# Optimization experiments

Measured on AMD Instinct MI355X. Metric: run time of the kernel, lower is better.

The kernel has to match this reference:

```python
import jax, jax.numpy as jnp
import numpy as np

N_HEAD = 16


def setup_inputs() -> dict:
    key = jax.random.key(0)
    ks = jax.random.split(key, 4)
    B, S, E = 1, 4096, 1024
    x = jax.random.normal(ks[0], (B, S, E), dtype=jnp.float32)
    # causal mask: True where attention is DISALLOWED (upper triangle)
    masked_matrix = ~jnp.tril(jnp.ones((S, S), dtype=bool))[None, None]
    Wqkv = jax.random.normal(ks[1], (E, 3 * E), dtype=jnp.float32) * (1.0 / np.sqrt(E))
    bqkv = jnp.zeros((3 * E,), dtype=jnp.float32)
    Wp = jax.random.normal(ks[2], (E, E), dtype=jnp.float32) * (1.0 / np.sqrt(E))
    bp = jnp.zeros((E,), dtype=jnp.float32)
    return {"x": x, "masked_matrix": masked_matrix, "Wqkv": Wqkv, "bqkv": bqkv,
            "Wp": Wp, "bp": bp}


def reference(x, masked_matrix, Wqkv, bqkv, Wp, bp):
    B, S, E = x.shape
    H = N_HEAD
    D = E // H
    qkv = x @ Wqkv + bqkv                        # [B,S,3E]
    q, k, v = jnp.split(qkv, 3, axis=-1)
    q = q.reshape(B, S, H, D).transpose(0, 2, 1, 3)  # [B,H,S,D]
    k = k.reshape(B, S, H, D).transpose(0, 2, 1, 3)
    v = v.reshape(B, S, H, D).transpose(0, 2, 1, 3)
    # NOTE: source applies NO 1/sqrt(D) scaling — kept faithful.
    att = jnp.einsum('bhqd,bhkd->bhqk', q, k)    # [B,H,S,S]
    att = jnp.where(masked_matrix, jnp.float32(-jnp.inf), att)
    att = jax.nn.softmax(att, axis=-1)
    res = jnp.einsum('bhqk,bhkd->bhqd', att, v)  # [B,H,S,D]
    res = res.transpose(0, 2, 1, 3).reshape(B, S, E)
    return res @ Wp + bp
```

## Files before the change

kernel.cpp:

```cpp
#include <hip/hip_runtime.h>
#include <hip/hip_bf16.h>
#include <math.h>

#define S_LEN 4096
#define EMB   1024
#define NHEAD 16
#define HDIM  64

typedef __attribute__((ext_vector_type(8))) _Float16 half8;
typedef __attribute__((ext_vector_type(4))) _Float16 half4;
typedef __attribute__((ext_vector_type(4))) float float4_t;
typedef __attribute__((ext_vector_type(16))) float float16_t;
typedef __attribute__((ext_vector_type(4))) int int4_t;
typedef __attribute__((ext_vector_type(2))) int int2_t;

#define GLOBAL_AS(p) ((const __attribute__((address_space(1))) void*)(p))
#define LDS_AS(p)    ((__attribute__((address_space(3))) void*)(p))

#define LOG2E 1.4426950408889634f

__global__ __launch_bounds__(256) void prep(
    const float* __restrict__ x, const float* __restrict__ Wqkv,
    const float* __restrict__ Wp,
    _Float16* __restrict__ xh, _Float16* __restrict__ WTh,
    _Float16* __restrict__ WpT)
{
    const int bid = blockIdx.x;
    if (bid < 4096) {
        const int i = bid * 256 + threadIdx.x;
        const float4_t v = ((const float4_t*)x)[i];
        half4 hh;
#pragma unroll
        for (int j = 0; j < 4; ++j) hh[j] = (_Float16)v[j];
        ((half4*)xh)[i] = hh;
        return;
    }
    __shared__ float t[64][65];
    const float* in;
    _Float16* out;
    int R, C, bx, by;
    if (bid < 4096 + 768) {
        const int idx = bid - 4096;
        bx = idx % 48; by = idx / 48;
        in = Wqkv; out = WTh; R = 1024; C = 3072;
    } else {
        const int idx = bid - 4864;
        bx = idx & 15; by = idx >> 4;
        in = Wp; out = WpT; R = 1024; C = 1024;
    }
    const int r0 = by * 64, c0 = bx * 64;
    for (int i = threadIdx.x; i < 64 * 64; i += 256) {
        int r = i >> 6, c = i & 63;
        t[r][c] = in[(size_t)(r0 + r) * C + c0 + c];
    }
    __syncthreads();
    for (int i = threadIdx.x; i < 64 * 64; i += 256) {
        int c = i >> 6, r = i & 63;
        out[(size_t)(c0 + c) * R + r0 + r] = (_Float16)t[r][c];
    }
}

__global__ __launch_bounds__(256) void gemm_qkv(
    const _Float16* __restrict__ Ag, const _Float16* __restrict__ Bg,
    const float* __restrict__ bias,
    _Float16* __restrict__ qk, _Float16* __restrict__ vt, int K)
{
    constexpr int BK = 32;
    __shared__ _Float16 Ah[128 * BK];
    __shared__ _Float16 Bh[128 * BK];

    const int tid = threadIdx.x;
    const int wave = tid >> 6, lane = tid & 63;
    const int l16 = lane & 15, quad = lane >> 4;
    const int wr = wave >> 1, wc = wave & 1;
    const int row0 = blockIdx.y * 128, col0 = blockIdx.x * 128;
    const int lrow = lane >> 2, lc8 = (lane & 3) * 8;

    float4_t acc[4][4];
#pragma unroll
    for (int i = 0; i < 4; ++i)
#pragma unroll
        for (int j = 0; j < 4; ++j) acc[i][j] = (float4_t){0.f, 0.f, 0.f, 0.f};

    for (int k0 = 0; k0 < K; k0 += BK) {
        __syncthreads();
#pragma unroll
        for (int i = 0; i < 2; ++i) {
            const int ar = i * 64 + wave * 16;
            __builtin_amdgcn_global_load_lds(
                GLOBAL_AS(Ag + (size_t)(row0 + ar + lrow) * K + k0 + lc8),
                LDS_AS(&Ah[ar * BK]), 16, 0, 0);
            __builtin_amdgcn_global_load_lds(
                GLOBAL_AS(Bg + (size_t)(col0 + ar + lrow) * K + k0 + lc8),
                LDS_AS(&Bh[ar * BK]), 16, 0, 0);
        }
        __syncthreads();

        half8 af[4], bfr[4];
#pragma unroll
        for (int t = 0; t < 4; ++t) {
            af[t]  = *(const half8*)&Ah[(wr * 64 + t * 16 + l16) * BK + quad * 8];
            bfr[t] = *(const half8*)&Bh[(wc * 64 + t * 16 + l16) * BK + quad * 8];
        }
#pragma unroll
        for (int i = 0; i < 4; ++i)
#pragma unroll
            for (int j = 0; j < 4; ++j)
                acc[i][j] = __builtin_amdgcn_mfma_f32_16x16x32_f16(af[i], bfr[j], acc[i][j], 0, 0, 0);
    }

#pragma unroll
    for (int i = 0; i < 4; ++i) {
#pragma unroll
        for (int j = 0; j < 4; ++j) {
            const int colb = col0 + wc * 64 + j * 16 + l16;
            const float bv = bias[colb];
            const int rowb = row0 + wr * 64 + i * 16 + quad * 4;
            if (colb < 2048) {
                const float sc = (colb >= 1024) ? LOG2E : 1.0f;
#pragma unroll
                for (int r = 0; r < 4; ++r)
                    qk[(size_t)(rowb + r) * 2048 + colb] =
                        (_Float16)((acc[i][j][r] + bv) * sc);
            } else {
                half4 w;
#pragma unroll
                for (int r = 0; r < 4; ++r) w[r] = (_Float16)(acc[i][j][r] + bv);
                *(half4*)&vt[(size_t)(colb - 2048) * 4096 + rowb] = w;
            }
        }
    }
}

__global__ __launch_bounds__(256) void gemm_out(
    const _Float16* __restrict__ Ag, const _Float16* __restrict__ Bg,
    const float* __restrict__ bias, float* __restrict__ C, int N, int K)
{
    constexpr int BK = 32;
    __shared__ _Float16 Ah[128 * BK];
    __shared__ _Float16 Bh[64 * BK];

    const int tid = threadIdx.x;
    const int wave = tid >> 6, lane = tid & 63;
    const int l16 = lane & 15, quad = lane >> 4;
    const int row0 = blockIdx.y * 128, col0 = blockIdx.x * 64;
    const int lrow = lane >> 2, lc8 = (lane & 3) * 8;

    float4_t acc[2][4];
#pragma unroll
    for (int i = 0; i < 2; ++i)
#pragma unroll
        for (int j = 0; j < 4; ++j) acc[i][j] = (float4_t){0.f, 0.f, 0.f, 0.f};

    for (int k0 = 0; k0 < K; k0 += BK) {
        __syncthreads();
#pragma unroll
        for (int i = 0; i < 2; ++i) {
            const int ar = i * 64 + wave * 16;
            __builtin_amdgcn_global_load_lds(
                GLOBAL_AS(Ag + (size_t)(row0 + ar + lrow) * K + k0 + lc8),
                LDS_AS(&Ah[ar * BK]), 16, 0, 0);
        }
        {
            const int br = wave * 16;
            __builtin_amdgcn_global_load_lds(
                GLOBAL_AS(Bg + (size_t)(col0 + br + lrow) * K + k0 + lc8),
                LDS_AS(&Bh[br * BK]), 16, 0, 0);
        }
        __syncthreads();

        half8 af[2], bfr[4];
#pragma unroll
        for (int t = 0; t < 2; ++t)
            af[t] = *(const half8*)&Ah[(wave * 32 + t * 16 + l16) * BK + quad * 8];
#pragma unroll
        for (int t = 0; t < 4; ++t)
            bfr[t] = *(const half8*)&Bh[(t * 16 + l16) * BK + quad * 8];
#pragma unroll
        for (int i = 0; i < 2; ++i)
#pragma unroll
            for (int j = 0; j < 4; ++j)
                acc[i][j] = __builtin_amdgcn_mfma_f32_16x16x32_f16(af[i], bfr[j], acc[i][j], 0, 0, 0);
    }

#pragma unroll
    for (int i = 0; i < 2; ++i) {
#pragma unroll
        for (int j = 0; j < 4; ++j) {
            const int colb = col0 + j * 16 + l16;
            const float bv = bias[colb];
#pragma unroll
            for (int r = 0; r < 4; ++r) {
                const int row = row0 + wave * 32 + i * 16 + quad * 4 + r;
                C[(size_t)row * N + colb] = acc[i][j][r] + bv;
            }
        }
    }
}

__global__ __launch_bounds__(256, 2) void flash_attn_f16(
    const _Float16* __restrict__ qk, const _Float16* __restrict__ v_t,
    _Float16* __restrict__ resh)
{
    __shared__ __align__(16) _Float16 KsT[2][64 * 64];
    __shared__ __align__(16) _Float16 VtT[2][64 * 64];

    const int bid  = blockIdx.x;
    const int h    = (bid & 7) * 2 + ((bid >> 3) & 1);
    const int s_   = bid >> 4;
    const int tile = (s_ < 16) ? (31 - s_) : (s_ - 16);
    const int wave = threadIdx.x >> 6;
    const int lane = threadIdx.x & 63;
    const int l31  = lane & 31;
    const int hi   = lane >> 5;

    const int dma_r = wave * 16 + (lane >> 3);
    const int dma_c = ((lane & 7) ^ (lane >> 3)) * 8;

    const _Float16* kplane = qk + 1024 + h * HDIM;
    const _Float16* vplane = v_t + (size_t)h * HDIM * 4096;

    const int q0      = tile * 128 + wave * 32;
    const int kb_last = tile * 128 + 64;

    half8 qf[4];
#pragma unroll
    for (int j = 0; j < 4; ++j)
        qf[j] = *(const half8*)(qk + (size_t)(q0 + l31) * 2048 + h * HDIM
                                + j * 16 + hi * 8);

    float16_t o0 = (float16_t)0.f, o1 = (float16_t)0.f;
    float m_r = -INFINITY, l_r = 0.f;

#pragma unroll
    for (int p = 0; p < 2; ++p) {
        const int r = dma_r + p * 8;
        __builtin_amdgcn_global_load_lds(
            GLOBAL_AS(kplane + (size_t)r * 2048 + dma_c),
            LDS_AS(&KsT[0][(wave * 128 + p * 64) * 8]), 16, 0, 0);
        __builtin_amdgcn_global_load_lds(
            GLOBAL_AS(vplane + (size_t)r * 4096 + dma_c),
            LDS_AS(&VtT[0][(wave * 128 + p * 64) * 8]), 16, 0, 0);
    }

    int ib = 0;
    for (int kb = 0; kb <= kb_last; kb += 64, ib ^= 1) {
        __syncthreads();

        if (kb < kb_last) {
            const int kn = kb + 64;
#pragma unroll
            for (int p = 0; p < 2; ++p) {
                const int r = dma_r + p * 8;
                __builtin_amdgcn_global_load_lds(
                    GLOBAL_AS(kplane + (size_t)(kn + r) * 2048 + dma_c),
                    LDS_AS(&KsT[ib ^ 1][(wave * 128 + p * 64) * 8]), 16, 0, 0);
                __builtin_amdgcn_global_load_lds(
                    GLOBAL_AS(vplane + (size_t)r * 4096 + kn + dma_c),
                    LDS_AS(&VtT[ib ^ 1][(wave * 128 + p * 64) * 8]), 16, 0, 0);
            }
        }

        if (kb <= q0 + 31) {
            float16_t s0 = (float16_t)0.f, s1 = (float16_t)0.f;
            __builtin_amdgcn_s_setprio(1);
#pragma unroll
            for (int j = 0; j < 4; ++j) {
                const int r7 = l31 & 7;
                const half8 kf0 = *(const half8*)&KsT[ib][
                    ((l31) * 8 + ((2 * j + hi) ^ r7)) * 8];
                const half8 kf1 = *(const half8*)&KsT[ib][
                    ((32 + l31) * 8 + ((2 * j + hi) ^ r7)) * 8];
                s0 = __builtin_amdgcn_mfma_f32_32x32x16_f16(kf0, qf[j], s0, 0, 0, 0);
                s1 = __builtin_amdgcn_mfma_f32_32x32x16_f16(kf1, qf[j], s1, 0, 0, 0);
            }
            __builtin_amdgcn_s_setprio(0);

            if (kb + 63 > q0) {
                const int qg = q0 + l31;
#pragma unroll
                for (int g = 0; g < 4; ++g)
#pragma unroll
                    for (int r = 0; r < 4; ++r) {
                        const int keyb = kb + r + 8 * g + 4 * hi;
                        if (keyb > qg)      s0[4 * g + r] = -INFINITY;
                        if (keyb + 32 > qg) s1[4 * g + r] = -INFINITY;
                    }
            }

            float mx = s0[0];
#pragma unroll
            for (int i = 1; i < 16; ++i) mx = fmaxf(mx, s0[i]);
#pragma unroll
            for (int i = 0; i < 16; ++i) mx = fmaxf(mx, s1[i]);
            mx = fmaxf(mx, __shfl_xor(mx, 32));
            const bool  grow  = mx > m_r + 8.0f;
            const float mnew  = grow ? mx : m_r;
            const float alpha = __builtin_amdgcn_exp2f(m_r - mnew);

            int w0[8], w1[8];
            float lsum = 0.f;
#pragma unroll
            for (int i = 0; i < 8; ++i) {
                const float pa = __builtin_amdgcn_exp2f(s0[2 * i]     - mnew);
                const float pb = __builtin_amdgcn_exp2f(s0[2 * i + 1] - mnew);
                lsum += pa + pb;
                w0[i] = __builtin_bit_cast(int, __builtin_amdgcn_cvt_pkrtz(pa, pb));
            }
#pragma unroll
            for (int i = 0; i < 8; ++i) {
                const float pa = __builtin_amdgcn_exp2f(s1[2 * i]     - mnew);
                const float pb = __builtin_amdgcn_exp2f(s1[2 * i + 1] - mnew);
                lsum += pa + pb;
                w1[i] = __builtin_bit_cast(int, __builtin_amdgcn_cvt_pkrtz(pa, pb));
            }
            l_r = l_r * alpha + lsum;
            m_r = mnew;
            if (__any(grow)) {
#pragma unroll
                for (int i = 0; i < 16; ++i) { o0[i] *= alpha; o1[i] *= alpha; }
            }

            half8 pf[4];
            {
                const int2_t a02 = __builtin_amdgcn_permlane32_swap(w0[0], w0[2], 0, 0);
                const int2_t a13 = __builtin_amdgcn_permlane32_swap(w0[1], w0[3], 0, 0);
                const int2_t a46 = __builtin_amdgcn_permlane32_swap(w0[4], w0[6], 0, 0);
                const int2_t a57 = __builtin_amdgcn_permlane32_swap(w0[5], w0[7], 0, 0);
                int4_t f0 = {a02[0], a13[0], a02[1], a13[1]};
                int4_t f1 = {a46[0], a57[0], a46[1], a57[1]};
                pf[0] = __builtin_bit_cast(half8, f0);
                pf[1] = __builtin_bit_cast(half8, f1);
                const int2_t b02 = __builtin_amdgcn_permlane32_swap(w1[0], w1[2], 0, 0);
                const int2_t b13 = __builtin_amdgcn_permlane32_swap(w1[1], w1[3], 0, 0);
                const int2_t b46 = __builtin_amdgcn_permlane32_swap(w1[4], w1[6], 0, 0);
                const int2_t b57 = __builtin_amdgcn_permlane32_swap(w1[5], w1[7], 0, 0);
                int4_t f2 = {b02[0], b13[0], b02[1], b13[1]};
                int4_t f3 = {b46[0], b57[0], b46[1], b57[1]};
                pf[2] = __builtin_bit_cast(half8, f2);
                pf[3] = __builtin_bit_cast(half8, f3);
            }

            __builtin_amdgcn_s_setprio(1);
#pragma unroll
            for (int kc = 0; kc < 4; ++kc) {
                const int r7 = l31 & 7;
                const half8 vf0 = *(const half8*)&VtT[ib][
                    ((l31) * 8 + ((2 * kc + hi) ^ r7)) * 8];
                const half8 vf1 = *(const half8*)&VtT[ib][
                    ((32 + l31) * 8 + ((2 * kc + hi) ^ r7)) * 8];
                o0 = __builtin_amdgcn_mfma_f32_32x32x16_f16(vf0, pf[kc], o0, 0, 0, 0);
                o1 = __builtin_amdgcn_mfma_f32_32x32x16_f16(vf1, pf[kc], o1, 0, 0, 0);
            }
            __builtin_amdgcn_s_setprio(0);
        }
    }

    float lr = l_r + __shfl_xor(l_r, 32);
    const float inv = 1.0f / lr;
#pragma unroll
    for (int g = 0; g < 4; ++g) {
        half4 wa, wb;
#pragma unroll
        for (int r = 0; r < 4; ++r) {
            wa[r] = (_Float16)(o0[4 * g + r] * inv);
            wb[r] = (_Float16)(o1[4 * g + r] * inv);
        }
        const size_t base = (size_t)(q0 + l31) * EMB + h * HDIM + 8 * g + 4 * hi;
        *(half4*)&resh[base]      = wa;
        *(half4*)&resh[base + 32] = wb;
    }
}

extern "C" void kernel_launch(void* const* d_in, const int* in_sizes, int n_in,
                              void* d_out, int out_size, void* d_ws, size_t ws_size,
                              hipStream_t stream)
{
    const float* x    = (const float*)d_in[0];
    const float* Wqkv = (const float*)d_in[2];
    const float* bqkv = (const float*)d_in[3];
    const float* Wp   = (const float*)d_in[4];
    const float* bp   = (const float*)d_in[5];
    float* out = (float*)d_out;

    _Float16* xh  = (_Float16*)d_ws;
    _Float16* WTh = xh + (size_t)4096 * 1024;
    _Float16* qkh = WTh + (size_t)3072 * 1024;
    _Float16* vtg = qkh + (size_t)4096 * 2048;
    _Float16* WpT = vtg + (size_t)1024 * 4096;
    _Float16* resh = xh;

    dim3 blk(256);

    prep<<<dim3(5120), blk, 0, stream>>>(x, Wqkv, Wp, xh, WTh, WpT);

    gemm_qkv<<<dim3(3072 / 128, 4096 / 128), blk, 0, stream>>>(
        xh, WTh, bqkv, qkh, vtg, 1024);

    flash_attn_f16<<<dim3(512), dim3(256), 0, stream>>>(qkh, vtg, resh);

    gemm_out<<<dim3(1024 / 64, 4096 / 128), blk, 0, stream>>>(
        resh, WpT, bp, out, 1024, 1024);
}
```

Measured before the change: 263.8 us.

## Split causal flash attention across two key-parity halves with a combine pass

Each query tile's key blocks are split into two interleaved halves (even and odd 64-key blocks), one per workgroup. This doubles the grid to 1024 blocks and raises the occupancy hint to 4 blocks per CU. Each half writes an unnormalized fp16 partial output plus its running max and sum, and a new combine kernel merges them with log-sum-exp rescaling. The aim is better occupancy and load balance across CUs on MI355X. The cost is extra global traffic for the partials, an additional kernel launch, and fp16 rounding of the unnormalized partial accumulators.

```diff
diff --git a/kernel.cpp b/kernel.cpp
--- a/kernel.cpp
+++ b/kernel.cpp
@@ -198,17 +198,22 @@
     }
 }
 
-__global__ __launch_bounds__(256, 2) void flash_attn_f16(
+__global__ __launch_bounds__(256, 4) void flash_attn_f16(
     const _Float16* __restrict__ qk, const _Float16* __restrict__ v_t,
-    _Float16* __restrict__ resh)
+    _Float16* __restrict__ opart, float* __restrict__ mlpart)
 {
     __shared__ __align__(16) _Float16 KsT[2][64 * 64];
     __shared__ __align__(16) _Float16 VtT[2][64 * 64];
 
     const int bid  = blockIdx.x;
-    const int h    = (bid & 7) * 2 + ((bid >> 3) & 1);
-    const int s_   = bid >> 4;
-    const int tile = (s_ < 16) ? (31 - s_) : (s_ - 16);
+    const int g    = bid & 255;
+    const int hv   = g & 15;
+    const int h    = (hv & 7) * 2 + (hv >> 3);
+    const int j    = g >> 4;
+    const int v    = bid >> 8;
+    const int tile = (v & 1) ? (31 - j) : j;
+    const int split= v >> 1;
+
     const int wave = threadIdx.x >> 6;
     const int lane = threadIdx.x & 63;
     const int l31  = lane & 31;
@@ -220,35 +225,36 @@
     const _Float16* kplane = qk + 1024 + h * HDIM;
     const _Float16* vplane = v_t + (size_t)h * HDIM * 4096;
 
-    const int q0      = tile * 128 + wave * 32;
-    const int kb_last = tile * 128 + 64;
+    const int q0 = tile * 128 + wave * 32;
 
     half8 qf[4];
 #pragma unroll
-    for (int j = 0; j < 4; ++j)
-        qf[j] = *(const half8*)(qk + (size_t)(q0 + l31) * 2048 + h * HDIM
-                                + j * 16 + hi * 8);
+    for (int jj = 0; jj < 4; ++jj)
+        qf[jj] = *(const half8*)(qk + (size_t)(q0 + l31) * 2048 + h * HDIM
+                                 + jj * 16 + hi * 8);
 
     float16_t o0 = (float16_t)0.f, o1 = (float16_t)0.f;
     float m_r = -INFINITY, l_r = 0.f;
 
+    const int kb0 = 64 * split;
 #pragma unroll
     for (int p = 0; p < 2; ++p) {
         const int r = dma_r + p * 8;
         __builtin_amdgcn_global_load_lds(
-            GLOBAL_AS(kplane + (size_t)r * 2048 + dma_c),
+            GLOBAL_AS(kplane + (size_t)(kb0 + r) * 2048 + dma_c),
             LDS_AS(&KsT[0][(wave * 128 + p * 64) * 8]), 16, 0, 0);
         __builtin_amdgcn_global_load_lds(
-            GLOBAL_AS(vplane + (size_t)r * 4096 + dma_c),
+            GLOBAL_AS(vplane + (size_t)r * 4096 + kb0 + dma_c),
             LDS_AS(&VtT[0][(wave * 128 + p * 64) * 8]), 16, 0, 0);
     }
 
     int ib = 0;
-    for (int kb = 0; kb <= kb_last; kb += 64, ib ^= 1) {
+    int kb = kb0;
+    for (int it = 0; it <= tile; ++it, kb += 128, ib ^= 1) {
         __syncthreads();
 
-        if (kb < kb_last) {
-            const int kn = kb + 64;
+        if (it < tile) {
+            const int kn = kb + 128;
 #pragma unroll
             for (int p = 0; p < 2; ++p) {
                 const int r = dma_r + p * 8;
@@ -265,26 +271,26 @@
             float16_t s0 = (float16_t)0.f, s1 = (float16_t)0.f;
             __builtin_amdgcn_s_setprio(1);
 #pragma unroll
-            for (int j = 0; j < 4; ++j) {
+            for (int jj = 0; jj < 4; ++jj) {
                 const int r7 = l31 & 7;
                 const half8 kf0 = *(const half8*)&KsT[ib][
-                    ((l31) * 8 + ((2 * j + hi) ^ r7)) * 8];
+                    ((l31) * 8 + ((2 * jj + hi) ^ r7)) * 8];
                 const half8 kf1 = *(const half8*)&KsT[ib][
-                    ((32 + l31) * 8 + ((2 * j + hi) ^ r7)) * 8];
-                s0 = __builtin_amdgcn_mfma_f32_32x32x16_f16(kf0, qf[j], s0, 0, 0, 0);
-                s1 = __builtin_amdgcn_mfma_f32_32x32x16_f16(kf1, qf[j], s1, 0, 0, 0);
+                    ((32 + l31) * 8 + ((2 * jj + hi) ^ r7)) * 8];
+                s0 = __builtin_amdgcn_mfma_f32_32x32x16_f16(kf0, qf[jj], s0, 0, 0, 0);
+                s1 = __builtin_amdgcn_mfma_f32_32x32x16_f16(kf1, qf[jj], s1, 0, 0, 0);
             }
             __builtin_amdgcn_s_setprio(0);
 
             if (kb + 63 > q0) {
                 const int qg = q0 + l31;
 #pragma unroll
-                for (int g = 0; g < 4; ++g)
+                for (int gg = 0; gg < 4; ++gg)
 #pragma unroll
                     for (int r = 0; r < 4; ++r) {
-                        const int keyb = kb + r + 8 * g + 4 * hi;
-                        if (keyb > qg)      s0[4 * g + r] = -INFINITY;
-                        if (keyb + 32 > qg) s1[4 * g + r] = -INFINITY;
+                        const int keyb = kb + r + 8 * gg + 4 * hi;
+                        if (keyb > qg)      s0[4 * gg + r] = -INFINITY;
+                        if (keyb + 32 > qg) s1[4 * gg + r] = -INFINITY;
                     }
             }
 
@@ -356,20 +362,47 @@
         }
     }
 
-    float lr = l_r + __shfl_xor(l_r, 32);
-    const float inv = 1.0f / lr;
-#pragma unroll
-    for (int g = 0; g < 4; ++g) {
+    const float lr = l_r + __shfl_xor(l_r, 32);
+    const size_t prow = (size_t)(split * 4096 + q0 + l31);
+#pragma unroll
+    for (int gg = 0; gg < 4; ++gg) {
         half4 wa, wb;
 #pragma unroll
         for (int r = 0; r < 4; ++r) {
-            wa[r] = (_Float16)(o0[4 * g + r] * inv);
-            wb[r] = (_Float16)(o1[4 * g + r] * inv);
-        }
-        const size_t base = (size_t)(q0 + l31) * EMB + h * HDIM + 8 * g + 4 * hi;
-        *(half4*)&resh[base]      = wa;
-        *(half4*)&resh[base + 32] = wb;
-    }
+            wa[r] = (_Float16)o0[4 * gg + r];
+            wb[r] = (_Float16)o1[4 * gg + r];
+        }
+        const size_t base = prow * 1024 + h * HDIM + 8 * gg + 4 * hi;
+        *(half4*)&opart[base]      = wa;
+        *(half4*)&opart[base + 32] = wb;
+    }
+    if (hi == 0) {
+        float2 ml; ml.x = m_r; ml.y = lr;
+        ((float2*)mlpart)[prow * 16 + h] = ml;
+    }
+}
+
+__global__ __launch_bounds__(256) void combine(
+    const _Float16* __restrict__ opart, const float* __restrict__ mlpart,
+    _Float16* __restrict__ resh)
+{
+    const int idx = blockIdx.x * 256 + threadIdx.x;
+    const int row = idx >> 7;
+    const int c8  = (idx & 127) * 8;
+    const int h   = c8 >> 6;
+    const float2 ml0 = ((const float2*)mlpart)[(size_t)row * 16 + h];
+    const float2 ml1 = ((const float2*)mlpart)[(size_t)(4096 + row) * 16 + h];
+    const float m  = fmaxf(ml0.x, ml1.x);
+    const float a0 = __builtin_amdgcn_exp2f(ml0.x - m);
+    const float a1 = __builtin_amdgcn_exp2f(ml1.x - m);
+    const float inv = 1.0f / (ml0.y * a0 + ml1.y * a1);
+    const half8 o0 = *(const half8*)&opart[(size_t)row * 1024 + c8];
+    const half8 o1 = *(const half8*)&opart[(size_t)(4096 + row) * 1024 + c8];
+    half8 w;
+#pragma unroll
+    for (int jj = 0; jj < 8; ++jj)
+        w[jj] = (_Float16)(((float)o0[jj] * a0 + (float)o1[jj] * a1) * inv);
+    *(half8*)&resh[(size_t)row * 1024 + c8] = w;
 }
 
 extern "C" void kernel_launch(void* const* d_in, const int* in_sizes, int n_in,
@@ -388,6 +421,8 @@
     _Float16* qkh = WTh + (size_t)3072 * 1024;
     _Float16* vtg = qkh + (size_t)4096 * 2048;
     _Float16* WpT = vtg + (size_t)1024 * 4096;
+    _Float16* opart = WpT + (size_t)1024 * 1024;
+    float* mlpart = (float*)(opart + (size_t)2 * 4096 * 1024);
     _Float16* resh = xh;
 
     dim3 blk(256);
@@ -397,7 +432,9 @@
     gemm_qkv<<<dim3(3072 / 128, 4096 / 128), blk, 0, stream>>>(
         xh, WTh, bqkv, qkh, vtg, 1024);
 
-    flash_attn_f16<<<dim3(512), dim3(256), 0, stream>>>(qkh, vtg, resh);
+    flash_attn_f16<<<dim3(1024), dim3(256), 0, stream>>>(qkh, vtg, opart, mlpart);
+
+    combine<<<dim3(2048), blk, 0, stream>>>(opart, mlpart, resh);
 
     gemm_out<<<dim3(1024 / 64, 4096 / 128), blk, 0, stream>>>(
         resh, WpT, bp, out, 1024, 1024);
```

Measured after the change: 245.6 us. 1.07x faster.
